# Kernel optimization log

Hardware: AMD Instinct MI355X
Metric: run time of the kernel (lower is better)

Reference implementation:

```python
import jax, jax.numpy as jnp
import numpy as np

N_E = 16384
E_DIM = 256
BETA = 0.25


def setup_inputs() -> dict:
    key = jax.random.key(0)
    k1, k2 = jax.random.split(key)
    z = jax.random.normal(k1, (8, E_DIM, 32, 32), dtype=jnp.float32)
    embedding = jax.random.uniform(
        k2, (N_E, E_DIM), dtype=jnp.float32, minval=-1.0 / N_E, maxval=1.0 / N_E
    )
    return {"z": z, "embedding": embedding}


def reference(z, embedding):
    # b c h w -> b h w c
    zc = jnp.transpose(z, (0, 2, 3, 1))
    b, h, w, c = zc.shape
    z_flat = zc.reshape(-1, c)  # [N, e_dim]

    # squared-distance matrix: ||z||^2 + ||e||^2 - 2 z e^T  -> [N, n_e]
    d = (
        jnp.sum(z_flat * z_flat, axis=1, keepdims=True)
        + jnp.sum(embedding * embedding, axis=1)
        - 2.0 * jnp.einsum("nd,kd->nk", z_flat, embedding)
    )
    idx = jnp.argmin(d, axis=1)  # [N]

    z_q = embedding[idx].reshape(b, h, w, c)

    sg = jax.lax.stop_gradient
    # legacy=True loss: mse(sg(z_q), z) + beta * mse(z_q, sg(z))
    loss = jnp.mean((sg(z_q) - zc) ** 2) + BETA * jnp.mean((z_q - sg(zc)) ** 2)

    # straight-through estimator
    z_q_st = zc + sg(z_q - zc)
    z_q_out = jnp.transpose(z_q_st, (0, 3, 1, 2))  # b h w c -> b c h w
    return z_q_out, loss, idx
```

## Files before the change

### kernel.cpp

```cpp
#include <hip/hip_runtime.h>

#define E_DIM  256
#define N_E    16384
#define N_ROWS 8192
#define HW     1024
#define NPART  128

typedef _Float16 f16x8 __attribute__((ext_vector_type(8)));
typedef float    f32x4 __attribute__((ext_vector_type(4)));

#define ESCALE   1048576.0f
#define UNSCALE  1.9073486328125e-6f

#define ROR_DPP(v, CTRL) \
  ((unsigned)__builtin_amdgcn_update_dpp(0, (int)(v), (CTRL), 0xF, 0xF, false))

__device__ __forceinline__ void gld_lds16(_Float16* lds, const _Float16* g) {
  __builtin_amdgcn_global_load_lds(
      (__attribute__((address_space(1))) void*)(g),
      (__attribute__((address_space(3))) void*)(lds), 16, 0, 0);
}

__device__ __forceinline__ float score_ref32(const float* zr,
                                             const float* __restrict__ E,
                                             const float* __restrict__ eNorm,
                                             int idx, float zn) {
  const float4* e4p = (const float4*)(E + (size_t)idx * E_DIM);
  float d0 = 0.f, d1 = 0.f, d2 = 0.f, d3 = 0.f;
#pragma unroll 16
  for (int q = 0; q < 64; ++q) {
    float4 e4 = e4p[q];
    d0 = fmaf(zr[q * 4 + 0], e4.x, d0);
    d1 = fmaf(zr[q * 4 + 1], e4.y, d1);
    d2 = fmaf(zr[q * 4 + 2], e4.z, d2);
    d3 = fmaf(zr[q * 4 + 3], e4.w, d3);
  }
  float dot = (d0 + d1) + (d2 + d3);
  float base = zn + eNorm[idx];
  float td = 2.0f * dot;
  return base - td;
}

#define ZB_Z    256
#define EB_E    512
__global__ __launch_bounds__(256) void k_prep(const float* __restrict__ z,
                                              const float* __restrict__ E,
                                              _Float16* __restrict__ Ah,
                                              _Float16* __restrict__ Bh,
                                              float* __restrict__ eNorm,
                                              float* __restrict__ zNorm,
                                              float* __restrict__ zL1,
                                              float* __restrict__ out_loss) {
#pragma clang fp contract(off)
  const int bi = blockIdx.x, t = threadIdx.x;

  if (bi < ZB_Z) {
    __shared__ float sLZ[256][32];
    __shared__ float sN2[16][32];
    __shared__ float sL1[16][32];
    const int n0 = bi * 32;
    const int b = n0 >> 10, hw0 = n0 & 1023;

    {
      const int nl = t & 31, cs = t >> 5;
      const float* zb = z + (size_t)b * E_DIM * HW + hw0 + nl;
#pragma unroll 4
      for (int it = 0; it < 32; ++it) {
        int c = it * 8 + cs;
        sLZ[c][nl] = zb[(size_t)c * HW];
      }
    }
    __syncthreads();

    {
      const int nl = t & 31, seg = t >> 5;
      const int n = n0 + nl;
      const int perm = (n >> 1) & 3;
#pragma unroll
      for (int u = 0; u < 4; ++u) {
        const int c0 = seg * 32 + u * 8;
        f16x8 hh;
#pragma unroll
        for (int j = 0; j < 8; ++j) hh[j] = (_Float16)sLZ[c0 + j][nl];
        size_t dst = (size_t)seg * (N_ROWS * 32) + (size_t)n * 32 + (size_t)(u ^ perm) * 8;
        *(f16x8*)&Ah[dst] = hh;
      }
    }

#pragma unroll
    for (int it = 0; it < 2; ++it) {
      int task = it * 256 + t;
      int nl = task & 31, c16 = task >> 5;
      int h = c16 >> 3, j = c16 & 7;
      float r2 = 0.f, r1 = 0.f;
#pragma unroll
      for (int i = 0; i < 16; ++i) {
        float v = sLZ[h * 128 + i * 8 + j][nl];
        r2 = r2 + v * v;
        r1 = r1 + fabsf(v);
      }
      sN2[c16][nl] = r2;
      sL1[c16][nl] = r1;
    }
    __syncthreads();
    if (t < 32) {
      float q[16], p[16];
#pragma unroll
      for (int c16 = 0; c16 < 16; ++c16) { q[c16] = sN2[c16][t]; p[c16] = sL1[c16][t]; }
      float h0 = ((q[0] + q[1]) + (q[2] + q[3])) + ((q[4] + q[5]) + (q[6] + q[7]));
      float h1 = ((q[8] + q[9]) + (q[10] + q[11])) + ((q[12] + q[13]) + (q[14] + q[15]));
      zNorm[n0 + t] = h0 + h1;
      float g0 = ((p[0] + p[1]) + (p[2] + p[3])) + ((p[4] + p[5]) + (p[6] + p[7]));
      float g1 = ((p[8] + p[9]) + (p[10] + p[11])) + ((p[12] + p[13]) + (p[14] + p[15]));
      zL1[n0 + t] = g0 + g1;
    }
  } else {
    __shared__ float sNP[8][32];
    const int be = bi - ZB_Z;
    if (be == 0 && t == 0) out_loss[0] = 0.f;
    const int kc = t >> 5, rl = t & 31;
    const int k = be * 32 + rl;
    const int perm = (k >> 1) & 3;
    const float* src = E + (size_t)k * E_DIM + kc * 32;

    float4 v4[8];
#pragma unroll
    for (int u2 = 0; u2 < 8; ++u2) v4[u2] = ((const float4*)src)[u2];

    float nsum = 0.f;
    size_t base = (size_t)kc * (N_E * 32) + (size_t)k * 32;
#pragma unroll
    for (int u = 0; u < 4; ++u) {
      float v[8] = {v4[u * 2].x, v4[u * 2].y, v4[u * 2].z, v4[u * 2].w,
                    v4[u * 2 + 1].x, v4[u * 2 + 1].y, v4[u * 2 + 1].z, v4[u * 2 + 1].w};
      f16x8 hh;
#pragma unroll
      for (int j = 0; j < 8; ++j) {
        nsum = nsum + v[j] * v[j];
        hh[j] = (_Float16)(v[j] * ESCALE);
      }
      *(f16x8*)&Bh[base + (size_t)(u ^ perm) * 8] = hh;
    }
    sNP[kc][rl] = nsum;
    __syncthreads();
    if (t < 32) {
      float s = 0.f;
#pragma unroll
      for (int kc2 = 0; kc2 < 8; ++kc2) s += sNP[kc2][t];
      eNorm[be * 32 + t] = s;
    }
  }
}

__global__ __launch_bounds__(256, 4) void k_scores_mfma(
    const _Float16* __restrict__ Ah, const _Float16* __restrict__ Bh,
    const float* __restrict__ eNorm,
    unsigned* __restrict__ pK1, unsigned* __restrict__ pK2,
    unsigned* __restrict__ pK3) {
#pragma clang fp contract(off)
  __shared__ alignas(16) _Float16 As[2][128][32];
  __shared__ alignas(16) _Float16 Bs[2][128][32];

  const int mt = blockIdx.x, nt = blockIdx.y;
  const int m0 = mt * 128, n0 = nt * 128;

  const int t = threadIdx.x;
  const int lane = t & 63, w = t >> 6;
  const int tx = lane & 15, quad = lane >> 4;
  const int wr = w & 1, wc = w >> 1;
  const int wm = wr * 64, wn = wc * 64;
  const int swz = (quad ^ ((tx >> 1) & 3)) * 8;

  const _Float16* gstage;
  size_t plane;
  _Float16* ls0;
  if (w < 2) { gstage = Ah + (size_t)(m0 + w * 64) * 32;       plane = (size_t)N_ROWS * 32; ls0 = &As[0][w * 64][0]; }
  else       { gstage = Bh + (size_t)(n0 + (w - 2) * 64) * 32; plane = (size_t)N_E * 32;    ls0 = &Bs[0][(w - 2) * 64][0]; }
  gstage += lane * 8;

  f32x4 acc[4][4];
#pragma unroll
  for (int i = 0; i < 4; ++i)
#pragma unroll
    for (int j = 0; j < 4; ++j) acc[i][j] = (f32x4){0.f, 0.f, 0.f, 0.f};

#pragma unroll
  for (int c = 0; c < 4; ++c) gld_lds16(ls0 + c * 512, gstage + c * 512);
  __syncthreads();

  for (int kc = 0; kc < 8; ++kc) {
    const int buf = kc & 1;

    if (kc < 7) {
      _Float16* lpre = ls0 + (size_t)(buf ^ 1) * 4096;
      const _Float16* gpre = gstage + (size_t)(kc + 1) * plane;
#pragma unroll
      for (int c = 0; c < 4; ++c) gld_lds16(lpre + c * 512, gpre + c * 512);
      __builtin_amdgcn_sched_barrier(0);
    }

    f16x8 ah[4], bh[4];
#pragma unroll
    for (int i = 0; i < 4; ++i)
      ah[i] = *(const f16x8*)&As[buf][wm + i * 16 + tx][swz];
#pragma unroll
    for (int j = 0; j < 4; ++j)
      bh[j] = *(const f16x8*)&Bs[buf][wn + j * 16 + tx][swz];

    __builtin_amdgcn_s_setprio(1);
#pragma unroll
    for (int j = 0; j < 4; ++j)
#pragma unroll
      for (int i = 0; i < 4; ++i)
        acc[i][j] = __builtin_amdgcn_mfma_f32_16x16x32_f16(ah[i], bh[j], acc[i][j], 0, 0, 0);
    __builtin_amdgcn_s_setprio(0);

    __syncthreads();
  }

  float* sF  = (float*)&As[0][0][0];
  float* eNq = sF;
  unsigned* sK1 = (unsigned*)(sF + 128);
  unsigned* sK2 = sK1 + 256;
  unsigned* sK3 = sK2 + 256;
  if (t < 128) eNq[t] = fmaf(eNorm[n0 + t], 2097152.f, 131072.f);
  __syncthreads();

#pragma unroll
  for (int i = 0; i < 4; ++i) {
#pragma unroll
    for (int r = 0; r < 4; ++r) {
      const int rloc = wm + i * 16 + quad * 4 + r;
      unsigned k0, k1, k2, k3;
      {
        float tq0 = fmaf(acc[i][0][r], -4.0f, eNq[wn + 0 * 16 + tx]);
        float tq1 = fmaf(acc[i][1][r], -4.0f, eNq[wn + 1 * 16 + tx]);
        float tq2 = fmaf(acc[i][2][r], -4.0f, eNq[wn + 2 * 16 + tx]);
        float tq3 = fmaf(acc[i][3][r], -4.0f, eNq[wn + 3 * 16 + tx]);
        k0 = (((unsigned)tq0) << 14) | (unsigned)(n0 + wn + 0 * 16 + tx);
        k1 = (((unsigned)tq1) << 14) | (unsigned)(n0 + wn + 1 * 16 + tx);
        k2 = (((unsigned)tq2) << 14) | (unsigned)(n0 + wn + 2 * 16 + tx);
        k3 = (((unsigned)tq3) << 14) | (unsigned)(n0 + wn + 3 * 16 + tx);
      }
      unsigned a = min(k0, k1), b = max(k0, k1);
      unsigned c = min(k2, k3), d = max(k2, k3);
      unsigned m1 = min(a, c), e = max(a, c);
      unsigned f = min(b, d);
      unsigned m2 = min(e, f), m3 = max(e, f);
#define MERGE_R(CTRL)                                              \
      {                                                            \
        unsigned o1 = ROR_DPP(m1, CTRL);                           \
        unsigned o2 = ROR_DPP(m2, CTRL);                           \
        unsigned o3 = ROR_DPP(m3, CTRL);                           \
        unsigned n1 = min(m1, o1);                                 \
        unsigned n2 = min(max(m1, o1), min(m2, o2));               \
        unsigned n3 = min(min(m3, o3), min(max(m2, o1), max(m1, o2))); \
        m1 = n1; m2 = n2; m3 = n3;                                 \
      }
      MERGE_R(0x121)
      MERGE_R(0x122)
      MERGE_R(0x124)
      MERGE_R(0x128)
#undef MERGE_R
      if (tx == 0) {
        sK1[wc * 128 + rloc] = m1;
        sK2[wc * 128 + rloc] = m2;
        sK3[wc * 128 + rloc] = m3;
      }
    }
  }
  __syncthreads();
  if (t < 128) {
    unsigned a1 = sK1[t], a2 = sK2[t], a3 = sK3[t];
    unsigned b1 = sK1[128 + t], b2 = sK2[128 + t], b3 = sK3[128 + t];
    const size_t o = (size_t)nt * N_ROWS + m0 + t;
    pK1[o] = min(a1, b1);
    pK2[o] = min(max(a1, b1), min(a2, b2));
    pK3[o] = min(min(a3, b3), min(max(a2, b1), max(a1, b2)));
  }
}

__global__ __launch_bounds__(1024) void k_post(
    const unsigned* __restrict__ pK1, const unsigned* __restrict__ pK2,
    const unsigned* __restrict__ pK3,
    const float* __restrict__ zL1, const float* __restrict__ zNorm,
    const float* __restrict__ z, const float* __restrict__ E,
    const float* __restrict__ eNorm,
    float* __restrict__ out, float* __restrict__ out_loss,
    float* __restrict__ out_idx) {
#pragma clang fp contract(off)
  __shared__ float zc[32][264];
  __shared__ unsigned sM[32][32];
  __shared__ unsigned gK[32];
  __shared__ int   fI[32];
  __shared__ int   cand[32][16];
  __shared__ int   ccnt[32];
  __shared__ int   heavy[32][4];
  __shared__ int   hcnt[32];
  __shared__ float fS[32][32];
  __shared__ int   fiS[32][32];
  __shared__ float wsum[16];

  const int t = threadIdx.x;
  const int r = t & 31, s = t >> 5;
  const int n0 = blockIdx.x * 32;
  const int n = n0 + r;
  const int b = n >> 10, hw = n & 1023;

  if (t < 32) { ccnt[t] = 0; hcnt[t] = 0; }

  {
    const float* zrow = z + ((size_t)b * E_DIM + s * 8) * HW + hw;
#pragma unroll
    for (int k = 0; k < 8; ++k) zc[r][s * 8 + k] = zrow[(size_t)k * HW];
  }

  unsigned mk = 0xFFFFFFFFu;
#pragma unroll
  for (int i = 0; i < 4; ++i) {
    int ti = s * 4 + i;
    mk = min(mk, pK1[(size_t)ti * N_ROWS + n]);
  }
  sM[s][r] = mk;
  __syncthreads();
  if (t < 32) {
    unsigned bk = sM[0][t];
#pragma unroll
    for (int s3 = 1; s3 < 32; ++s3) bk = min(bk, sM[s3][t]);
    gK[t] = bk;
  }
  __syncthreads();

  {
    const unsigned qW =
        (unsigned)(fmaf(zL1[n], 2.384185791015625e-7f, 8e-5f) * 2097152.f) + 3u;
    unsigned thrq = (gK[r] >> 14) + qW;
    if (thrq > 262143u) thrq = 262143u;
    const unsigned thrk = (thrq << 14) | 0x3FFFu;
#pragma unroll
    for (int i = 0; i < 4; ++i) {
      int ti = s * 4 + i;
      size_t o = (size_t)ti * N_ROWS + n;
      unsigned k1 = pK1[o], k2 = pK2[o], k3 = pK3[o];
      if (k1 <= thrk) { int p = atomicAdd(&ccnt[r], 1); if (p < 16) cand[r][p] = (int)(k1 & 0x3FFFu); }
      if (k2 <= thrk) { int p = atomicAdd(&ccnt[r], 1); if (p < 16) cand[r][p] = (int)(k2 & 0x3FFFu); }
      if (k3 <= thrk) { int p = atomicAdd(&hcnt[r], 1); if (p < 4)  heavy[r][p] = ti; }
    }
  }
  __syncthreads();

  {
    const int rcnt = ccnt[r], rhc = hcnt[r];
    const bool ovf = (rcnt > 16) || (rhc > 4);
    const bool ex = (rcnt > 1) || (rhc > 0);
    float bv = 3.4e38f;
    int bi = 0x7fffffff;
    if (ex) {
      const float zn = zNorm[n];
      if (ovf) {
        for (int k = s; k < N_E; k += 32) {
          float sp = score_ref32(&zc[r][0], E, eNorm, k, zn);
          if (sp < bv || (sp == bv && k < bi)) { bv = sp; bi = k; }
        }
      } else {
        for (int c = s; c < rcnt; c += 32) {
          int idx = cand[r][c];
          float sp = score_ref32(&zc[r][0], E, eNorm, idx, zn);
          if (sp < bv || (sp == bv && idx < bi)) { bv = sp; bi = idx; }
        }
        for (int h = 0; h < rhc; ++h) {
          int ti = heavy[r][h];
          for (int cc = s; cc < 128; cc += 32) {
            int idx = ti * 128 + cc;
            float sp = score_ref32(&zc[r][0], E, eNorm, idx, zn);
            if (sp < bv || (sp == bv && idx < bi)) { bv = sp; bi = idx; }
          }
        }
      }
    }
    fS[r][s] = bv;
    fiS[r][s] = bi;
  }
  __syncthreads();
  if (t < 32) {
    const int rcnt = ccnt[t], rhc = hcnt[t];
    int fidx;
    if (rcnt <= 1 && rhc == 0) {
      fidx = (int)(gK[t] & 0x3FFFu);
    } else {
      float bv = fS[t][0];
      int bi = fiS[t][0];
#pragma unroll
      for (int s3 = 1; s3 < 32; ++s3) {
        float v = fS[t][s3];
        int id = fiS[t][s3];
        if (v < bv || (v == bv && id < bi)) { bv = v; bi = id; }
      }
      fidx = bi;
    }
    fI[t] = fidx;
    out_idx[n0 + t] = (float)fidx;
  }
  __syncthreads();

  const int idx = fI[r];
  const float4* erow4 = (const float4*)(E + (size_t)idx * E_DIM + s * 8);
  float* orow = out + ((size_t)b * E_DIM + s * 8) * HW + hw;
  float acc = 0.f;
#pragma unroll
  for (int c4 = 0; c4 < 2; ++c4) {
    float4 e4 = erow4[c4];
    float ev[4] = {e4.x, e4.y, e4.z, e4.w};
#pragma unroll
    for (int j2 = 0; j2 < 4; ++j2) {
      int c = c4 * 4 + j2;
      float zv = zc[r][s * 8 + c];
      orow[(size_t)c * HW] = ev[j2];
      float d = ev[j2] - zv;
      acc = fmaf(d, d, acc);
    }
  }
  for (int off = 32; off > 0; off >>= 1) acc += __shfl_down(acc, off, 64);
  if ((t & 63) == 0) wsum[t >> 6] = acc;
  __syncthreads();
  if (t == 0) {
    float s0 = 0.f;
#pragma unroll
    for (int wv = 0; wv < 16; ++wv) s0 += wsum[wv];
    atomicAdd(out_loss, s0 * (1.25f / 2097152.f));
  }
}

extern "C" void kernel_launch(void* const* d_in, const int* in_sizes, int n_in,
                              void* d_out, int out_size, void* d_ws, size_t ws_size,
                              hipStream_t stream) {
  const float* z = (const float*)d_in[0];
  const float* E = (const float*)d_in[1];
  float* out = (float*)d_out;
  float* out_loss = out + 2097152;
  float* out_idx = out + 2097153;

  _Float16* Ah = (_Float16*)d_ws;
  _Float16* Bh = Ah + (size_t)N_ROWS * E_DIM;
  float* eNorm = (float*)(Bh + (size_t)N_E * E_DIM);
  float* zL1 = eNorm + N_E;
  float* zNorm = zL1 + N_ROWS;
  unsigned* pK1 = (unsigned*)(zNorm + N_ROWS);
  unsigned* pK2 = pK1 + (size_t)NPART * N_ROWS;
  unsigned* pK3 = pK2 + (size_t)NPART * N_ROWS;

  k_prep<<<ZB_Z + EB_E, 256, 0, stream>>>(z, E, Ah, Bh, eNorm, zNorm, zL1, out_loss);
  k_scores_mfma<<<dim3(N_ROWS / 128, N_E / 128), 256, 0, stream>>>(
      Ah, Bh, eNorm, pK1, pK2, pK3);
  k_post<<<N_ROWS / 32, 1024, 0, stream>>>(
      pK1, pK2, pK3, zL1, zNorm, z, E, eNorm, out, out_loss, out_idx);
}
```

Before: 205.3 us.

## Load MFMA operands directly from global memory instead of LDS staging

The score GEMM kernel stops staging A and B tiles in double-buffered LDS through global_load_lds. Each wave now reads its f16x8 fragments straight from global memory, with the k-loop fully unrolled and no per-iteration barriers. The epilogue scratch gets its own small shared arrays, and launch bounds drop to 2 blocks per CU so more registers can hold the in-flight loads. This removes LDS traffic and synchronisation, but every fragment is fetched from global/L2 by each wave that needs it (B is reused by both row-waves, A by both column-waves), and occupancy may fall.

```diff
diff --git a/kernel.cpp b/kernel.cpp
--- a/kernel.cpp
+++ b/kernel.cpp
@@ -14,12 +14,6 @@
 
 #define ROR_DPP(v, CTRL) \
   ((unsigned)__builtin_amdgcn_update_dpp(0, (int)(v), (CTRL), 0xF, 0xF, false))
-
-__device__ __forceinline__ void gld_lds16(_Float16* lds, const _Float16* g) {
-  __builtin_amdgcn_global_load_lds(
-      (__attribute__((address_space(1))) void*)(g),
-      (__attribute__((address_space(3))) void*)(lds), 16, 0, 0);
-}
 
 __device__ __forceinline__ float score_ref32(const float* zr,
                                              const float* __restrict__ E,
@@ -152,14 +146,16 @@
   }
 }
 
-__global__ __launch_bounds__(256, 4) void k_scores_mfma(
+__global__ __launch_bounds__(256, 2) void k_scores_mfma(
     const _Float16* __restrict__ Ah, const _Float16* __restrict__ Bh,
     const float* __restrict__ eNorm,
     unsigned* __restrict__ pK1, unsigned* __restrict__ pK2,
     unsigned* __restrict__ pK3) {
 #pragma clang fp contract(off)
-  __shared__ alignas(16) _Float16 As[2][128][32];
-  __shared__ alignas(16) _Float16 Bs[2][128][32];
+  __shared__ float eNq[128];
+  __shared__ unsigned sK1[256];
+  __shared__ unsigned sK2[256];
+  __shared__ unsigned sK3[256];
 
   const int mt = blockIdx.x, nt = blockIdx.y;
   const int m0 = mt * 128, n0 = nt * 128;
@@ -171,12 +167,11 @@
   const int wm = wr * 64, wn = wc * 64;
   const int swz = (quad ^ ((tx >> 1) & 3)) * 8;
 
-  const _Float16* gstage;
-  size_t plane;
-  _Float16* ls0;
-  if (w < 2) { gstage = Ah + (size_t)(m0 + w * 64) * 32;       plane = (size_t)N_ROWS * 32; ls0 = &As[0][w * 64][0]; }
-  else       { gstage = Bh + (size_t)(n0 + (w - 2) * 64) * 32; plane = (size_t)N_E * 32;    ls0 = &Bs[0][(w - 2) * 64][0]; }
-  gstage += lane * 8;
+  const size_t planeA = (size_t)N_ROWS * 32, planeB = (size_t)N_E * 32;
+  const size_t baseA = (size_t)(m0 + wm + tx) * 32 + swz;
+  const size_t baseB = (size_t)(n0 + wn + tx) * 32 + swz;
+
+  if (t < 128) eNq[t] = fmaf(eNorm[n0 + t], 2097152.f, 131072.f);
 
   f32x4 acc[4][4];
 #pragma unroll
@@ -185,27 +180,14 @@
     for (int j = 0; j < 4; ++j) acc[i][j] = (f32x4){0.f, 0.f, 0.f, 0.f};
 
 #pragma unroll
-  for (int c = 0; c < 4; ++c) gld_lds16(ls0 + c * 512, gstage + c * 512);
-  __syncthreads();
-
   for (int kc = 0; kc < 8; ++kc) {
-    const int buf = kc & 1;
-
-    if (kc < 7) {
-      _Float16* lpre = ls0 + (size_t)(buf ^ 1) * 4096;
-      const _Float16* gpre = gstage + (size_t)(kc + 1) * plane;
-#pragma unroll
-      for (int c = 0; c < 4; ++c) gld_lds16(lpre + c * 512, gpre + c * 512);
-      __builtin_amdgcn_sched_barrier(0);
-    }
-
     f16x8 ah[4], bh[4];
 #pragma unroll
     for (int i = 0; i < 4; ++i)
-      ah[i] = *(const f16x8*)&As[buf][wm + i * 16 + tx][swz];
+      ah[i] = *(const f16x8*)&Ah[kc * planeA + baseA + (size_t)i * 512];
 #pragma unroll
     for (int j = 0; j < 4; ++j)
-      bh[j] = *(const f16x8*)&Bs[buf][wn + j * 16 + tx][swz];
+      bh[j] = *(const f16x8*)&Bh[kc * planeB + baseB + (size_t)j * 512];
 
     __builtin_amdgcn_s_setprio(1);
 #pragma unroll
@@ -214,16 +196,8 @@
       for (int i = 0; i < 4; ++i)
         acc[i][j] = __builtin_amdgcn_mfma_f32_16x16x32_f16(ah[i], bh[j], acc[i][j], 0, 0, 0);
     __builtin_amdgcn_s_setprio(0);
-
-    __syncthreads();
-  }
-
-  float* sF  = (float*)&As[0][0][0];
-  float* eNq = sF;
-  unsigned* sK1 = (unsigned*)(sF + 128);
-  unsigned* sK2 = sK1 + 256;
-  unsigned* sK3 = sK2 + 256;
-  if (t < 128) eNq[t] = fmaf(eNorm[n0 + t], 2097152.f, 131072.f);
+  }
+
   __syncthreads();
 
 #pragma unroll
```

Result: faster. 183.4 us (-10.7%).
